# Performance work log

Measured on AMD Instinct MI355X. Metric: run time of the kernel, lower is better.

Reference implementation:

```python
import jax, jax.numpy as jnp
import numpy as np

N = 50000
E = 800000
D = 128
L = 2


def setup_inputs() -> dict:
    key = jax.random.key(0)
    k0, k1, k2 = jax.random.split(key, 3)
    x = jax.random.normal(k0, (N, D), dtype=jnp.float32)
    edge_index = jax.random.randint(k1, (2, E), 0, N, dtype=jnp.int64)
    # GCNConv weights: one [D, D] matrix + bias per layer (dim_in -> dim_in)
    W = jax.random.normal(k2, (L, D, D), dtype=jnp.float32) * (1.0 / np.sqrt(D))
    b = jnp.zeros((L, D), dtype=jnp.float32)
    return {"x": x, "edge_index": edge_index, "W": W, "b": b}


def reference(x, edge_index, W, b):
    """Stacked GCNConv + relu (dropout is identity in eval mode).

    GCNConv: out = D^{-1/2} (A + I) D^{-1/2} (X W) + b, with self-loops added.
    """
    n = x.shape[0]
    loops = jnp.arange(n, dtype=edge_index.dtype)
    src = jnp.concatenate([edge_index[0], loops])  # [E + N]
    dst = jnp.concatenate([edge_index[1], loops])  # [E + N]
    # Degree (with self-loops) based symmetric normalization
    deg = jax.ops.segment_sum(jnp.ones_like(dst, dtype=x.dtype), dst, num_segments=n)
    dinv = jax.lax.rsqrt(deg)  # deg >= 1 thanks to self-loops
    coef = (dinv[src] * dinv[dst])[:, None]  # [E + N, 1]

    num_layers = W.shape[0]
    for i in range(num_layers):
        h = x @ W[i]  # transform first, as PyG GCNConv does
        x = jax.ops.segment_sum(h[src] * coef, dst, num_segments=n) + b[i]
        x = jax.nn.relu(x)
        # F.dropout with training=False is identity
    return x
```

## Files before the change

kernel.cpp:

```cpp
#include <hip/hip_runtime.h>
#include <hip/hip_fp16.h>


#define D 128
#define WP 136
#define YP 136
#define ABI 8
#define AGT 32
#define NB_SCAN 196

typedef _Float16 half8 __attribute__((ext_vector_type(8)));
typedef float floatx4 __attribute__((ext_vector_type(4)));


__global__ void count_kernel(const int* __restrict__ src,
                             const int* __restrict__ dst, int* deg8,
                             int* __restrict__ rank, int e, int n) {
    int i = blockIdx.x * blockDim.x + threadIdx.x;
    if (i < e) {
        int c = (src[i] >> 13) * n;
        rank[i] = atomicAdd(&deg8[c + dst[i]], 1);
    }
}

__global__ __launch_bounds__(256) void scanA_cvtw_kernel(const int* __restrict__ deg8,
                                                         int* __restrict__ degT,
                                                         int* __restrict__ base8,
                                                         int* __restrict__ partial,
                                                         int n, int nbs,
                                                         const float* __restrict__ W,
                                                         __half* __restrict__ WhT) {
    __shared__ int red[4];
    int tid = threadIdx.x;
    int bid = blockIdx.x;
    if (bid < nbs) {
        int i = bid * 256 + tid;
        int tot = 0;
        if (i < n) {
            int run = 0;
#pragma unroll
            for (int c = 0; c < 8; ++c) {
                base8[c * n + i] = run;
                run += deg8[c * n + i];
            }
            degT[i] = run;
            tot = run;
        }
        for (int off = 32; off > 0; off >>= 1) tot += __shfl_down(tot, off, 64);
        if ((tid & 63) == 0) red[tid >> 6] = tot;
        __syncthreads();
        if (tid == 0) partial[bid] = red[0] + red[1] + red[2] + red[3];
    } else {
        int id = (bid - nbs) * 256 + tid;
        int l = id >> 14;
        int rem = id & 16383;
        int f = rem >> 7;
        int k = rem & 127;
        WhT[id] = __float2half(W[l * 16384 + k * 128 + f]);
    }
}

__global__ __launch_bounds__(256) void scanC2_kernel(const int* __restrict__ degT,
                                                     const int* __restrict__ partial,
                                                     int* __restrict__ row_ptr,
                                                     float* __restrict__ dinv, int n) {
    __shared__ int sc[256];
    __shared__ int scb[256];
    int tid = threadIdx.x;
    int bid = blockIdx.x;
    int p = (tid < NB_SCAN) ? partial[tid] : 0;
    scb[tid] = p;
    __syncthreads();
    for (int off = 1; off < 256; off <<= 1) {
        int v = (tid >= off) ? scb[tid - off] : 0;
        __syncthreads();
        scb[tid] += v;
        __syncthreads();
    }
    int i = bid * 256 + tid;
    int c = (i < n) ? degT[i] : 0;
    sc[tid] = c;
    __syncthreads();
    for (int off = 1; off < 256; off <<= 1) {
        int v = (tid >= off) ? sc[tid - off] : 0;
        __syncthreads();
        sc[tid] += v;
        __syncthreads();
    }
    if (i < n) {
        int base = ((bid == 0) ? 0 : scb[bid - 1]) + sc[tid] - c;
        row_ptr[i] = base;
        dinv[i] = rsqrtf((float)(c + 1));
    }
    if (bid == 0 && tid == 0) row_ptr[n] = scb[NB_SCAN - 1];
}


__device__ inline void gemm_body(int bid, int tid,
                                 const float* __restrict__ Xf,
                                 const __half* __restrict__ WhT,
                                 __half* __restrict__ Hh, int n,
                                 _Float16* wlds) {
#pragma unroll
    for (int q = 0; q < 8; ++q) {
        int idx = tid + q * 256;
        int row = idx >> 4;
        int col8 = (idx & 15) * 8;
        const uint2* gsrc = (const uint2*)(WhT + row * 128 + col8);
        uint2 a = gsrc[0];
        uint2 b = gsrc[1];
        uint2* ldst = (uint2*)(wlds + row * WP + col8);
        ldst[0] = a;
        ldst[1] = b;
    }
    __syncthreads();

    const int wave = tid >> 6;
    const int lane = tid & 63;
    const int m = lane & 15;
    const int quad = lane >> 4;

    const int node = bid * 64 + wave * 16 + m;
    const int node_ld = node < n ? node : (n - 1);

    half8 bfr[4];
#pragma unroll
    for (int k = 0; k < 4; ++k) {
        const float4* p = (const float4*)(Xf + (size_t)node_ld * 128 + k * 32 + quad * 8);
        float4 lo = p[0];
        float4 hi = p[1];
        half8 h;
        h[0] = (_Float16)lo.x; h[1] = (_Float16)lo.y;
        h[2] = (_Float16)lo.z; h[3] = (_Float16)lo.w;
        h[4] = (_Float16)hi.x; h[5] = (_Float16)hi.y;
        h[6] = (_Float16)hi.z; h[7] = (_Float16)hi.w;
        bfr[k] = h;
    }

    floatx4 acc[8];
#pragma unroll
    for (int f = 0; f < 8; ++f) acc[f] = (floatx4){0.f, 0.f, 0.f, 0.f};

#pragma unroll
    for (int f = 0; f < 8; ++f) {
#pragma unroll
        for (int k = 0; k < 4; ++k) {
            half8 a = *(const half8*)(wlds + (f * 16 + m) * WP + k * 32 + quad * 8);
            acc[f] = __builtin_amdgcn_mfma_f32_16x16x32_f16(a, bfr[k], acc[f], 0, 0, 0);
        }
    }

    if (node < n) {
#pragma unroll
        for (int f = 0; f < 8; ++f) {
            __half2 p0 = __floats2half2_rn(acc[f][0], acc[f][1]);
            __half2 p1 = __floats2half2_rn(acc[f][2], acc[f][3]);
            uint2 pk;
            pk.x = *(unsigned int*)&p0;
            pk.y = *(unsigned int*)&p1;
            *(uint2*)(Hh + (size_t)node * 128 + f * 16 + quad * 4) = pk;
        }
    }
}

__device__ inline void fill_body(int i,
                                 const int* __restrict__ src,
                                 const int* __restrict__ dst,
                                 const int* __restrict__ rank,
                                 const int* __restrict__ row_ptr,
                                 const int* __restrict__ base8,
                                 const float* __restrict__ dinv,
                                 int2* __restrict__ recs, int e, int n) {
    if (i < e) {
        int d = dst[i];
        int s = src[i];
        int c = s >> 13;
        int pos = row_ptr[d] + base8[c * n + d] + rank[i];
        int2 rec;
        rec.x = s;
        rec.y = __float_as_int(dinv[s] * dinv[d]);
        recs[pos] = rec;
    }
}


__global__ __launch_bounds__(256) void gemmfill_kernel(const float* __restrict__ Xf,
                                                       const __half* __restrict__ WhT,
                                                       __half* __restrict__ Hh, int n, int nbg,
                                                       const int* __restrict__ src,
                                                       const int* __restrict__ dst,
                                                       const int* __restrict__ rank,
                                                       const int* __restrict__ row_ptr,
                                                       const int* __restrict__ base8,
                                                       const float* __restrict__ dinv,
                                                       int2* __restrict__ recs, int e) {
    __shared__ _Float16 wlds[128 * WP];
    int bid = blockIdx.x;
    int tid = threadIdx.x;
    if (bid < nbg) {
        gemm_body(bid, tid, Xf, WhT, Hh, n, wlds);
    } else {
        fill_body((bid - nbg) * 256 + tid, src, dst, rank, row_ptr, base8, dinv, recs, e, n);
    }
}


__device__ inline void unpack8(uint4 u, float* f) {
    union { unsigned int x; __half2 h; } a, b, c, d;
    a.x = u.x; b.x = u.y; c.x = u.z; d.x = u.w;
    float2 f0 = __half22float2(a.h);
    float2 f1 = __half22float2(b.h);
    float2 f2 = __half22float2(c.h);
    float2 f3 = __half22float2(d.h);
    f[0] = f0.x; f[1] = f0.y; f[2] = f1.x; f[3] = f1.y;
    f[4] = f2.x; f[5] = f2.y; f[6] = f3.x; f[7] = f3.y;
}

__device__ inline void agg_row_q(int v, int fl,
                                 const uint4* __restrict__ H16,
                                 const int2* __restrict__ recs,
                                 const int* __restrict__ row_ptr,
                                 const float* __restrict__ dinv,
                                 float* acc) {
    {
        float di = dinv[v];
        float selfc = di * di;
        uint4 hv = H16[(size_t)v * 16 + fl];
        float f[8]; unpack8(hv, f);
#pragma unroll
        for (int t = 0; t < 8; ++t) acc[t] = f[t] * selfc;
    }

    int e0 = row_ptr[v];
    int e1 = row_ptr[v + 1];
    int e = e0;
    for (; e + ABI <= e1; e += ABI) {
        int2 r[ABI]; uint4 hu[ABI];
#pragma unroll
        for (int j = 0; j < ABI; ++j) r[j] = recs[e + j];
#pragma unroll
        for (int j = 0; j < ABI; ++j) hu[j] = H16[(size_t)r[j].x * 16 + fl];
#pragma unroll
        for (int j = 0; j < ABI; ++j) {
            float c = __int_as_float(r[j].y);
            float f[8]; unpack8(hu[j], f);
#pragma unroll
            for (int t = 0; t < 8; ++t) acc[t] = fmaf(f[t], c, acc[t]);
        }
    }
    if (e < e1) {
        int2 r[ABI]; uint4 hu[ABI]; bool act[ABI];
#pragma unroll
        for (int j = 0; j < ABI; ++j) {
            act[j] = (e + j) < e1;
            if (act[j]) r[j] = recs[e + j];
        }
#pragma unroll
        for (int j = 0; j < ABI; ++j) {
            if (act[j]) hu[j] = H16[(size_t)r[j].x * 16 + fl];
        }
#pragma unroll
        for (int j = 0; j < ABI; ++j) {
            if (act[j]) {
                float c = __int_as_float(r[j].y);
                float f[8]; unpack8(hu[j], f);
#pragma unroll
                for (int t = 0; t < 8; ++t) acc[t] = fmaf(f[t], c, acc[t]);
            }
        }
    }
}

__global__ __launch_bounds__(256, 4) void agg_kernel(const __half* __restrict__ H,
                                                     const int2* __restrict__ recs,
                                                     const int* __restrict__ row_ptr,
                                                     const float* __restrict__ dinv,
                                                     const float* __restrict__ bias,
                                                     float* __restrict__ YF, int n) {
    int wave = threadIdx.x >> 6;
    int lane = threadIdx.x & 63;
    int qw = lane >> 4;
    int fl = lane & 15;
    int v = blockIdx.x * 16 + wave * 4 + qw;
    if (v >= n) return;

    const uint4* H16 = (const uint4*)H;
    float acc[8];
    agg_row_q(v, fl, H16, recs, row_ptr, dinv, acc);

    const float4* B4 = (const float4*)bias;
    float4 b0 = B4[fl * 2];
    float4 b1 = B4[fl * 2 + 1];
    float4* Y4 = (float4*)YF;
    Y4[(size_t)v * 32 + fl * 2] = make_float4(
        fmaxf(acc[0] + b0.x, 0.f), fmaxf(acc[1] + b0.y, 0.f),
        fmaxf(acc[2] + b0.z, 0.f), fmaxf(acc[3] + b0.w, 0.f));
    Y4[(size_t)v * 32 + fl * 2 + 1] = make_float4(
        fmaxf(acc[4] + b1.x, 0.f), fmaxf(acc[5] + b1.y, 0.f),
        fmaxf(acc[6] + b1.z, 0.f), fmaxf(acc[7] + b1.w, 0.f));
}

__global__ __launch_bounds__(512, 4) void aggemm_kernel(
    const __half* __restrict__ H,
    const int2* __restrict__ recs,
    const int* __restrict__ row_ptr,
    const float* __restrict__ dinv,
    const float* __restrict__ bias,
    const __half* __restrict__ WhT2,
    __half* __restrict__ H2, int n) {
    __shared__ _Float16 yt[AGT * YP];
    const int tid = threadIdx.x;
    const int wave = tid >> 6;
    const int lane = tid & 63;
    const int qw = lane >> 4;
    const int fl = lane & 15;
    const int g = blockIdx.x;
    const uint4* H16 = (const uint4*)H;

    {
        const float4* B4 = (const float4*)bias;
        float4 b0 = B4[fl * 2];
        float4 b1 = B4[fl * 2 + 1];
        int r = wave * 4 + qw;
        int v = g * AGT + r;
        if (v < n) {
            float acc[8];
            agg_row_q(v, fl, H16, recs, row_ptr, dinv, acc);
            __half2 p0 = __floats2half2_rn(fmaxf(acc[0] + b0.x, 0.f), fmaxf(acc[1] + b0.y, 0.f));
            __half2 p1 = __floats2half2_rn(fmaxf(acc[2] + b0.z, 0.f), fmaxf(acc[3] + b0.w, 0.f));
            __half2 p2 = __floats2half2_rn(fmaxf(acc[4] + b1.x, 0.f), fmaxf(acc[5] + b1.y, 0.f));
            __half2 p3 = __floats2half2_rn(fmaxf(acc[6] + b1.z, 0.f), fmaxf(acc[7] + b1.w, 0.f));
            uint4 pk;
            pk.x = *(unsigned int*)&p0;
            pk.y = *(unsigned int*)&p1;
            pk.z = *(unsigned int*)&p2;
            pk.w = *(unsigned int*)&p3;
            *(uint4*)&yt[r * YP + fl * 8] = pk;
        } else {
            uint4 z = make_uint4(0, 0, 0, 0);
            *(uint4*)&yt[r * YP + fl * 8] = z;
        }
    }
    __syncthreads();

    const int mg = wave & 1;
    const int fh = wave >> 1;
    const int node = g * AGT + mg * 16 + fl;

    half8 bfr[4];
#pragma unroll
    for (int k = 0; k < 4; ++k)
        bfr[k] = *(const half8*)&yt[(mg * 16 + fl) * YP + k * 32 + qw * 8];

#pragma unroll
    for (int fb = 0; fb < 2; ++fb) {
        int f = fh * 2 + fb;
        floatx4 a4 = (floatx4){0.f, 0.f, 0.f, 0.f};
#pragma unroll
        for (int k = 0; k < 4; ++k) {
            half8 a = *(const half8*)(WhT2 + ((f * 16 + fl) * 128 + k * 32 + qw * 8));
            a4 = __builtin_amdgcn_mfma_f32_16x16x32_f16(a, bfr[k], a4, 0, 0, 0);
        }
        if (node < n) {
            __half2 p0 = __floats2half2_rn(a4[0], a4[1]);
            __half2 p1 = __floats2half2_rn(a4[2], a4[3]);
            uint2 pk;
            pk.x = *(unsigned int*)&p0;
            pk.y = *(unsigned int*)&p1;
            *(uint2*)(H2 + (size_t)node * 128 + f * 16 + qw * 4) = pk;
        }
    }
}


extern "C" void kernel_launch(void* const* d_in, const int* in_sizes, int n_in,
                              void* d_out, int out_size, void* d_ws, size_t ws_size,
                              hipStream_t stream) {
    const float* x = (const float*)d_in[0];
    const int* ei = (const int*)d_in[1];
    const float* W = (const float*)d_in[2];
    const float* b = (const float*)d_in[3];
    float* out = (float*)d_out;

    const int N = in_sizes[0] / D;
    const int E = in_sizes[1] / 2;

    const int* src = ei;
    const int* dst = ei + E;

    int* wsi = (int*)d_ws;
    float* wsf = (float*)d_ws;
    const size_t o_deg8 = 0;
    const size_t o_degT = o_deg8 + 400000;
    const size_t o_dinv = o_degT + 50000;
    const size_t o_rp   = o_dinv + 50000;
    const size_t o_part = o_rp + 50016;
    const size_t o_boff = o_part + 256;
    const size_t o_b8   = o_boff + 256;
    const size_t o_rank = o_b8 + 400000;
    const size_t o_rec  = o_rank + 800000;
    const size_t o_h    = o_rec + 1600000;
    const size_t o_wht  = o_h + 3200000;
    const size_t o_h2   = o_wht + 16384;

    int* deg8    = wsi + o_deg8;
    int* degT    = wsi + o_degT;
    float* dinv  = wsf + o_dinv;
    int* row_ptr = wsi + o_rp;
    int* partial = wsi + o_part;
    int* base8   = wsi + o_b8;
    int* rank    = wsi + o_rank;
    int2* recs   = (int2*)(wsi + o_rec);
    __half* h    = (__half*)(wsi + o_h);
    __half* wht  = (__half*)(wsi + o_wht);
    __half* h2   = (__half*)(wsi + o_h2);

    const int nb_e = (E + 255) / 256;
    const int nb_s = (N + 255) / 256;
    const int nb_g = (N + 63) / 64;
    const int nb_ag = (N + AGT - 1) / AGT;
    const int nb_a = (N + 15) / 16;

    hipMemsetAsync(deg8, 0, (size_t)8 * 50000 * sizeof(int), stream);
    count_kernel<<<nb_e, 256, 0, stream>>>(src, dst, deg8, rank, E, N);
    scanA_cvtw_kernel<<<nb_s + 128, 256, 0, stream>>>(deg8, degT, base8, partial,
                                                      N, nb_s, W, wht);
    scanC2_kernel<<<nb_s, 256, 0, stream>>>(degT, partial, row_ptr, dinv, N);
    gemmfill_kernel<<<nb_g + nb_e, 256, 0, stream>>>(x, wht, h, N, nb_g,
                                                     src, dst, rank, row_ptr, base8,
                                                     dinv, recs, E);
    aggemm_kernel<<<nb_ag, 512, 0, stream>>>(h, recs, row_ptr, dinv, b,
                                             wht + 16384, h2, N);
    agg_kernel<<<nb_a, 256, 0, stream>>>(h2, recs, row_ptr, dinv, b + D, out, N);
}
```

Measured before the change: 221.2 us.

## Aggregate node pairs in source-banded order with interleaved base offsets

Stores per-node band offsets in a node-major base9 array (8 offsets plus total), so each destination row's edges can be walked band by band by source-id range. Each 16-lane group now aggregates two nodes at once, interleaving their gathers. The aggemm kernel tile grows from 32 to 64 nodes, and the final layer uses a new 512-thread pair kernel. The aim is better L2 locality for H gathers, since concurrently processed rows touch similar source bands, plus more memory-level parallelism. In exchange there is more loop and band-boundary overhead, batches of 4 instead of 8, and possible divergence between the paired nodes.

```diff
diff --git a/kernel.cpp b/kernel.cpp
--- a/kernel.cpp
+++ b/kernel.cpp
@@ -5,8 +5,6 @@
 #define D 128
 #define WP 136
 #define YP 136
-#define ABI 8
-#define AGT 32
 #define NB_SCAN 196
 
 typedef _Float16 half8 __attribute__((ext_vector_type(8)));
@@ -25,7 +23,7 @@
 
 __global__ __launch_bounds__(256) void scanA_cvtw_kernel(const int* __restrict__ deg8,
                                                          int* __restrict__ degT,
-                                                         int* __restrict__ base8,
+                                                         int* __restrict__ base9,
                                                          int* __restrict__ partial,
                                                          int n, int nbs,
                                                          const float* __restrict__ W,
@@ -40,9 +38,10 @@
             int run = 0;
 #pragma unroll
             for (int c = 0; c < 8; ++c) {
-                base8[c * n + i] = run;
+                base9[(size_t)i * 9 + c] = run;
                 run += deg8[c * n + i];
             }
+            base9[(size_t)i * 9 + 8] = run;
             degT[i] = run;
             tot = run;
         }
@@ -168,14 +167,14 @@
                                  const int* __restrict__ dst,
                                  const int* __restrict__ rank,
                                  const int* __restrict__ row_ptr,
-                                 const int* __restrict__ base8,
+                                 const int* __restrict__ base9,
                                  const float* __restrict__ dinv,
                                  int2* __restrict__ recs, int e, int n) {
     if (i < e) {
         int d = dst[i];
         int s = src[i];
         int c = s >> 13;
-        int pos = row_ptr[d] + base8[c * n + d] + rank[i];
+        int pos = row_ptr[d] + base9[(size_t)d * 9 + c] + rank[i];
         int2 rec;
         rec.x = s;
         rec.y = __float_as_int(dinv[s] * dinv[d]);
@@ -191,7 +190,7 @@
                                                        const int* __restrict__ dst,
                                                        const int* __restrict__ rank,
                                                        const int* __restrict__ row_ptr,
-                                                       const int* __restrict__ base8,
+                                                       const int* __restrict__ base9,
                                                        const float* __restrict__ dinv,
                                                        int2* __restrict__ recs, int e) {
     __shared__ _Float16 wlds[128 * WP];
@@ -200,7 +199,7 @@
     if (bid < nbg) {
         gemm_body(bid, tid, Xf, WhT, Hh, n, wlds);
     } else {
-        fill_body((bid - nbg) * 256 + tid, src, dst, rank, row_ptr, base8, dinv, recs, e, n);
+        fill_body((bid - nbg) * 256 + tid, src, dst, rank, row_ptr, base9, dinv, recs, e, n);
     }
 }
 
@@ -216,99 +215,101 @@
     f[4] = f2.x; f[5] = f2.y; f[6] = f3.x; f[7] = f3.y;
 }
 
-__device__ inline void agg_row_q(int v, int fl,
-                                 const uint4* __restrict__ H16,
-                                 const int2* __restrict__ recs,
-                                 const int* __restrict__ row_ptr,
-                                 const float* __restrict__ dinv,
-                                 float* acc) {
-    {
-        float di = dinv[v];
-        float selfc = di * di;
-        uint4 hv = H16[(size_t)v * 16 + fl];
+__device__ inline void agg_pair_banded(int v0, int v1, int fl, int n,
+                                       const uint4* __restrict__ H16,
+                                       const int2* __restrict__ recs,
+                                       const int* __restrict__ row_ptr,
+                                       const int* __restrict__ base9,
+                                       const float* __restrict__ dinv,
+                                       float* a0, float* a1) {
+    const bool k0 = v0 < n, k1 = v1 < n;
+    const int rp0 = k0 ? row_ptr[v0] : 0;
+    const int rp1 = k1 ? row_ptr[v1] : 0;
+    const int* b0p = base9 + (size_t)(k0 ? v0 : 0) * 9;
+    const int* b1p = base9 + (size_t)(k1 ? v1 : 0) * 9;
+
+    if (k0) {
+        float di = dinv[v0];
+        float sc = di * di;
+        uint4 hv = H16[(size_t)v0 * 16 + fl];
         float f[8]; unpack8(hv, f);
 #pragma unroll
-        for (int t = 0; t < 8; ++t) acc[t] = f[t] * selfc;
-    }
-
-    int e0 = row_ptr[v];
-    int e1 = row_ptr[v + 1];
-    int e = e0;
-    for (; e + ABI <= e1; e += ABI) {
-        int2 r[ABI]; uint4 hu[ABI];
-#pragma unroll
-        for (int j = 0; j < ABI; ++j) r[j] = recs[e + j];
-#pragma unroll
-        for (int j = 0; j < ABI; ++j) hu[j] = H16[(size_t)r[j].x * 16 + fl];
-#pragma unroll
-        for (int j = 0; j < ABI; ++j) {
-            float c = __int_as_float(r[j].y);
-            float f[8]; unpack8(hu[j], f);
-#pragma unroll
-            for (int t = 0; t < 8; ++t) acc[t] = fmaf(f[t], c, acc[t]);
-        }
-    }
-    if (e < e1) {
-        int2 r[ABI]; uint4 hu[ABI]; bool act[ABI];
-#pragma unroll
-        for (int j = 0; j < ABI; ++j) {
-            act[j] = (e + j) < e1;
-            if (act[j]) r[j] = recs[e + j];
-        }
-#pragma unroll
-        for (int j = 0; j < ABI; ++j) {
-            if (act[j]) hu[j] = H16[(size_t)r[j].x * 16 + fl];
-        }
-#pragma unroll
-        for (int j = 0; j < ABI; ++j) {
-            if (act[j]) {
-                float c = __int_as_float(r[j].y);
-                float f[8]; unpack8(hu[j], f);
-#pragma unroll
-                for (int t = 0; t < 8; ++t) acc[t] = fmaf(f[t], c, acc[t]);
-            }
-        }
-    }
-}
-
-__global__ __launch_bounds__(256, 4) void agg_kernel(const __half* __restrict__ H,
-                                                     const int2* __restrict__ recs,
-                                                     const int* __restrict__ row_ptr,
-                                                     const float* __restrict__ dinv,
-                                                     const float* __restrict__ bias,
-                                                     float* __restrict__ YF, int n) {
-    int wave = threadIdx.x >> 6;
-    int lane = threadIdx.x & 63;
-    int qw = lane >> 4;
-    int fl = lane & 15;
-    int v = blockIdx.x * 16 + wave * 4 + qw;
-    if (v >= n) return;
-
-    const uint4* H16 = (const uint4*)H;
-    float acc[8];
-    agg_row_q(v, fl, H16, recs, row_ptr, dinv, acc);
-
-    const float4* B4 = (const float4*)bias;
-    float4 b0 = B4[fl * 2];
-    float4 b1 = B4[fl * 2 + 1];
-    float4* Y4 = (float4*)YF;
-    Y4[(size_t)v * 32 + fl * 2] = make_float4(
-        fmaxf(acc[0] + b0.x, 0.f), fmaxf(acc[1] + b0.y, 0.f),
-        fmaxf(acc[2] + b0.z, 0.f), fmaxf(acc[3] + b0.w, 0.f));
-    Y4[(size_t)v * 32 + fl * 2 + 1] = make_float4(
-        fmaxf(acc[4] + b1.x, 0.f), fmaxf(acc[5] + b1.y, 0.f),
-        fmaxf(acc[6] + b1.z, 0.f), fmaxf(acc[7] + b1.w, 0.f));
-}
-
-__global__ __launch_bounds__(512, 4) void aggemm_kernel(
+        for (int t = 0; t < 8; ++t) a0[t] = f[t] * sc;
+    } else {
+#pragma unroll
+        for (int t = 0; t < 8; ++t) a0[t] = 0.f;
+    }
+    if (k1) {
+        float di = dinv[v1];
+        float sc = di * di;
+        uint4 hv = H16[(size_t)v1 * 16 + fl];
+        float f[8]; unpack8(hv, f);
+#pragma unroll
+        for (int t = 0; t < 8; ++t) a1[t] = f[t] * sc;
+    } else {
+#pragma unroll
+        for (int t = 0; t < 8; ++t) a1[t] = 0.f;
+    }
+
+#pragma unroll 1
+    for (int c = 0; c < 8; ++c) {
+        int s0 = 0, e0 = 0, s1 = 0, e1 = 0;
+        if (k0) { s0 = rp0 + b0p[c]; e0 = rp0 + b0p[c + 1]; }
+        if (k1) { s1 = rp1 + b1p[c]; e1 = rp1 + b1p[c + 1]; }
+        while (s0 < e0 || s1 < e1) {
+            int2 r0[4], r1[4]; uint4 h0[4], h1[4];
+            bool c0[4], c1[4];
+#pragma unroll
+            for (int j = 0; j < 4; ++j) {
+                c0[j] = (s0 + j) < e0;
+                if (c0[j]) r0[j] = recs[s0 + j];
+            }
+#pragma unroll
+            for (int j = 0; j < 4; ++j) {
+                c1[j] = (s1 + j) < e1;
+                if (c1[j]) r1[j] = recs[s1 + j];
+            }
+#pragma unroll
+            for (int j = 0; j < 4; ++j) {
+                if (c0[j]) h0[j] = H16[(size_t)r0[j].x * 16 + fl];
+            }
+#pragma unroll
+            for (int j = 0; j < 4; ++j) {
+                if (c1[j]) h1[j] = H16[(size_t)r1[j].x * 16 + fl];
+            }
+#pragma unroll
+            for (int j = 0; j < 4; ++j) {
+                if (c0[j]) {
+                    float cf = __int_as_float(r0[j].y);
+                    float f[8]; unpack8(h0[j], f);
+#pragma unroll
+                    for (int t = 0; t < 8; ++t) a0[t] = fmaf(f[t], cf, a0[t]);
+                }
+            }
+#pragma unroll
+            for (int j = 0; j < 4; ++j) {
+                if (c1[j]) {
+                    float cf = __int_as_float(r1[j].y);
+                    float f[8]; unpack8(h1[j], f);
+#pragma unroll
+                    for (int t = 0; t < 8; ++t) a1[t] = fmaf(f[t], cf, a1[t]);
+                }
+            }
+            s0 += 4; s1 += 4;
+        }
+    }
+}
+
+__global__ __launch_bounds__(512, 3) void aggemm_kernel(
     const __half* __restrict__ H,
     const int2* __restrict__ recs,
     const int* __restrict__ row_ptr,
+    const int* __restrict__ base9,
     const float* __restrict__ dinv,
     const float* __restrict__ bias,
     const __half* __restrict__ WhT2,
     __half* __restrict__ H2, int n) {
-    __shared__ _Float16 yt[AGT * YP];
+    __shared__ _Float16 yt[64 * YP];
     const int tid = threadIdx.x;
     const int wave = tid >> 6;
     const int lane = tid & 63;
@@ -318,34 +319,48 @@
     const uint4* H16 = (const uint4*)H;
 
     {
+        const int q = wave * 4 + qw;
+        const int r0 = q * 2;
+        const int v0 = g * 64 + r0;
+        const int v1 = v0 + 1;
+        float a0[8], a1[8];
+        agg_pair_banded(v0, v1, fl, n, H16, recs, row_ptr, base9, dinv, a0, a1);
+
         const float4* B4 = (const float4*)bias;
-        float4 b0 = B4[fl * 2];
-        float4 b1 = B4[fl * 2 + 1];
-        int r = wave * 4 + qw;
-        int v = g * AGT + r;
-        if (v < n) {
-            float acc[8];
-            agg_row_q(v, fl, H16, recs, row_ptr, dinv, acc);
-            __half2 p0 = __floats2half2_rn(fmaxf(acc[0] + b0.x, 0.f), fmaxf(acc[1] + b0.y, 0.f));
-            __half2 p1 = __floats2half2_rn(fmaxf(acc[2] + b0.z, 0.f), fmaxf(acc[3] + b0.w, 0.f));
-            __half2 p2 = __floats2half2_rn(fmaxf(acc[4] + b1.x, 0.f), fmaxf(acc[5] + b1.y, 0.f));
-            __half2 p3 = __floats2half2_rn(fmaxf(acc[6] + b1.z, 0.f), fmaxf(acc[7] + b1.w, 0.f));
+        float4 bb0 = B4[fl * 2];
+        float4 bb1 = B4[fl * 2 + 1];
+        {
+            __half2 p0 = __floats2half2_rn(fmaxf(a0[0] + bb0.x, 0.f), fmaxf(a0[1] + bb0.y, 0.f));
+            __half2 p1 = __floats2half2_rn(fmaxf(a0[2] + bb0.z, 0.f), fmaxf(a0[3] + bb0.w, 0.f));
+            __half2 p2 = __floats2half2_rn(fmaxf(a0[4] + bb1.x, 0.f), fmaxf(a0[5] + bb1.y, 0.f));
+            __half2 p3 = __floats2half2_rn(fmaxf(a0[6] + bb1.z, 0.f), fmaxf(a0[7] + bb1.w, 0.f));
             uint4 pk;
             pk.x = *(unsigned int*)&p0;
             pk.y = *(unsigned int*)&p1;
             pk.z = *(unsigned int*)&p2;
             pk.w = *(unsigned int*)&p3;
-            *(uint4*)&yt[r * YP + fl * 8] = pk;
-        } else {
-            uint4 z = make_uint4(0, 0, 0, 0);
-            *(uint4*)&yt[r * YP + fl * 8] = z;
-        }
+            *(uint4*)&yt[r0 * YP + fl * 8] = pk;
+        }
+        {
+            __half2 p0 = __floats2half2_rn(fmaxf(a1[0] + bb0.x, 0.f), fmaxf(a1[1] + bb0.y, 0.f));
+            __half2 p1 = __floats2half2_rn(fmaxf(a1[2] + bb0.z, 0.f), fmaxf(a1[3] + bb0.w, 0.f));
+            __half2 p2 = __floats2half2_rn(fmaxf(a1[4] + bb1.x, 0.f), fmaxf(a1[5] + bb1.y, 0.f));
+            __half2 p3 = __floats2half2_rn(fmaxf(a1[6] + bb1.z, 0.f), fmaxf(a1[7] + bb1.w, 0.f));
+            uint4 pk;
+            pk.x = *(unsigned int*)&p0;
+            pk.y = *(unsigned int*)&p1;
+            pk.z = *(unsigned int*)&p2;
+            pk.w = *(unsigned int*)&p3;
+            *(uint4*)&yt[(r0 + 1) * YP + fl * 8] = pk;
+        }
+        if (v0 >= n) { uint4 z = make_uint4(0, 0, 0, 0); *(uint4*)&yt[r0 * YP + fl * 8] = z; }
+        if (v1 >= n) { uint4 z = make_uint4(0, 0, 0, 0); *(uint4*)&yt[(r0 + 1) * YP + fl * 8] = z; }
     }
     __syncthreads();
 
-    const int mg = wave & 1;
-    const int fh = wave >> 1;
-    const int node = g * AGT + mg * 16 + fl;
+    const int mg = wave & 3;
+    const int fh = wave >> 2;
+    const int node = g * 64 + mg * 16 + fl;
 
     half8 bfr[4];
 #pragma unroll
@@ -353,8 +368,8 @@
         bfr[k] = *(const half8*)&yt[(mg * 16 + fl) * YP + k * 32 + qw * 8];
 
 #pragma unroll
-    for (int fb = 0; fb < 2; ++fb) {
-        int f = fh * 2 + fb;
+    for (int fb = 0; fb < 4; ++fb) {
+        int f = fh * 4 + fb;
         floatx4 a4 = (floatx4){0.f, 0.f, 0.f, 0.f};
 #pragma unroll
         for (int k = 0; k < 4; ++k) {
@@ -369,6 +384,49 @@
             pk.y = *(unsigned int*)&p1;
             *(uint2*)(H2 + (size_t)node * 128 + f * 16 + qw * 4) = pk;
         }
+    }
+}
+
+__global__ __launch_bounds__(512, 3) void agg_out_kernel(
+    const __half* __restrict__ H,
+    const int2* __restrict__ recs,
+    const int* __restrict__ row_ptr,
+    const int* __restrict__ base9,
+    const float* __restrict__ dinv,
+    const float* __restrict__ bias,
+    float* __restrict__ YF, int n) {
+    const int tid = threadIdx.x;
+    const int wave = tid >> 6;
+    const int lane = tid & 63;
+    const int qw = lane >> 4;
+    const int fl = lane & 15;
+    const int q = wave * 4 + qw;
+    const int v0 = blockIdx.x * 64 + q * 2;
+    const int v1 = v0 + 1;
+    const uint4* H16 = (const uint4*)H;
+
+    float a0[8], a1[8];
+    agg_pair_banded(v0, v1, fl, n, H16, recs, row_ptr, base9, dinv, a0, a1);
+
+    const float4* B4 = (const float4*)bias;
+    float4 bb0 = B4[fl * 2];
+    float4 bb1 = B4[fl * 2 + 1];
+    float4* Y4 = (float4*)YF;
+    if (v0 < n) {
+        Y4[(size_t)v0 * 32 + fl * 2] = make_float4(
+            fmaxf(a0[0] + bb0.x, 0.f), fmaxf(a0[1] + bb0.y, 0.f),
+            fmaxf(a0[2] + bb0.z, 0.f), fmaxf(a0[3] + bb0.w, 0.f));
+        Y4[(size_t)v0 * 32 + fl * 2 + 1] = make_float4(
+            fmaxf(a0[4] + bb1.x, 0.f), fmaxf(a0[5] + bb1.y, 0.f),
+            fmaxf(a0[6] + bb1.z, 0.f), fmaxf(a0[7] + bb1.w, 0.f));
+    }
+    if (v1 < n) {
+        Y4[(size_t)v1 * 32 + fl * 2] = make_float4(
+            fmaxf(a1[0] + bb0.x, 0.f), fmaxf(a1[1] + bb0.y, 0.f),
+            fmaxf(a1[2] + bb0.z, 0.f), fmaxf(a1[3] + bb0.w, 0.f));
+        Y4[(size_t)v1 * 32 + fl * 2 + 1] = make_float4(
+            fmaxf(a1[4] + bb1.x, 0.f), fmaxf(a1[5] + bb1.y, 0.f),
+            fmaxf(a1[6] + bb1.z, 0.f), fmaxf(a1[7] + bb1.w, 0.f));
     }
 }
 
@@ -395,9 +453,8 @@
     const size_t o_dinv = o_degT + 50000;
     const size_t o_rp   = o_dinv + 50000;
     const size_t o_part = o_rp + 50016;
-    const size_t o_boff = o_part + 256;
-    const size_t o_b8   = o_boff + 256;
-    const size_t o_rank = o_b8 + 400000;
+    const size_t o_b9   = o_part + 256;
+    const size_t o_rank = o_b9 + 450048;
     const size_t o_rec  = o_rank + 800000;
     const size_t o_h    = o_rec + 1600000;
     const size_t o_wht  = o_h + 3200000;
@@ -408,7 +465,7 @@
     float* dinv  = wsf + o_dinv;
     int* row_ptr = wsi + o_rp;
     int* partial = wsi + o_part;
-    int* base8   = wsi + o_b8;
+    int* base9   = wsi + o_b9;
     int* rank    = wsi + o_rank;
     int2* recs   = (int2*)(wsi + o_rec);
     __half* h    = (__half*)(wsi + o_h);
@@ -418,18 +475,18 @@
     const int nb_e = (E + 255) / 256;
     const int nb_s = (N + 255) / 256;
     const int nb_g = (N + 63) / 64;
-    const int nb_ag = (N + AGT - 1) / AGT;
-    const int nb_a = (N + 15) / 16;
+    const int nb_a = (N + 63) / 64;
 
     hipMemsetAsync(deg8, 0, (size_t)8 * 50000 * sizeof(int), stream);
     count_kernel<<<nb_e, 256, 0, stream>>>(src, dst, deg8, rank, E, N);
-    scanA_cvtw_kernel<<<nb_s + 128, 256, 0, stream>>>(deg8, degT, base8, partial,
+    scanA_cvtw_kernel<<<nb_s + 128, 256, 0, stream>>>(deg8, degT, base9, partial,
                                                       N, nb_s, W, wht);
     scanC2_kernel<<<nb_s, 256, 0, stream>>>(degT, partial, row_ptr, dinv, N);
     gemmfill_kernel<<<nb_g + nb_e, 256, 0, stream>>>(x, wht, h, N, nb_g,
-                                                     src, dst, rank, row_ptr, base8,
+                                                     src, dst, rank, row_ptr, base9,
                                                      dinv, recs, E);
-    aggemm_kernel<<<nb_ag, 512, 0, stream>>>(h, recs, row_ptr, dinv, b,
-                                             wht + 16384, h2, N);
-    agg_kernel<<<nb_a, 256, 0, stream>>>(h2, recs, row_ptr, dinv, b + D, out, N);
-}
+    aggemm_kernel<<<nb_g, 512, 0, stream>>>(h, recs, row_ptr, base9, dinv, b,
+                                            wht + 16384, h2, N);
+    agg_out_kernel<<<nb_a, 512, 0, stream>>>(h2, recs, row_ptr, base9, dinv,
+                                             b + D, out, N);
+}
```

Result: slower. 291.3 us (+31.7%).
